# Optimization experiments

Measured on AMD Instinct MI355X. Metric: run time of the kernel, lower is better.

The kernel has to match this reference:

```python
import jax, jax.numpy as jnp
import numpy as np

H = 256   # hidden size
U = 10    # attention units


def _lstm_cell(xt, h, c, Wih, Whh, bih, bhh):
    # PyTorch gate order: i, f, g, o
    gates = xt @ Wih.T + h @ Whh.T + bih + bhh          # [B, 4H]
    i, f, g, o = jnp.split(gates, 4, axis=-1)
    i = jax.nn.sigmoid(i); f = jax.nn.sigmoid(f)
    g = jnp.tanh(g);       o = jax.nn.sigmoid(o)
    c = f * c + i * g
    h = o * jnp.tanh(c)
    return h, c


def setup_inputs() -> dict:
    key = jax.random.key(0)
    ks = jax.random.split(key, 12)
    B, S = 512, 256
    s = 1.0 / np.sqrt(H)
    x = jax.random.normal(ks[0], (B, S), dtype=jnp.float32)
    y = jax.random.randint(ks[1], (B, S), 0, S, dtype=jnp.int64)
    return {
        "x": x,
        "y": y,
        "enc_Wih": jax.random.uniform(ks[2], (4 * H, 1), jnp.float32, -s, s),
        "enc_Whh": jax.random.uniform(ks[3], (4 * H, H), jnp.float32, -s, s),
        "enc_bih": jax.random.uniform(ks[4], (4 * H,), jnp.float32, -s, s),
        "enc_bhh": jax.random.uniform(ks[5], (4 * H,), jnp.float32, -s, s),
        "dec_Wih": jax.random.uniform(ks[6], (4 * H, H + 1), jnp.float32, -s, s),
        "dec_Whh": jax.random.uniform(ks[7], (4 * H, H), jnp.float32, -s, s),
        "dec_bih": jax.random.uniform(ks[8], (4 * H,), jnp.float32, -s, s),
        "dec_bhh": jax.random.uniform(ks[9], (4 * H,), jnp.float32, -s, s),
        "att_W1": jax.random.uniform(ks[10], (U, H), jnp.float32, -s, s),
        "att_W2": jax.random.uniform(ks[11], (U, H), jnp.float32, -s, s),
        "att_V": jax.random.uniform(jax.random.fold_in(key, 99), (1, U), jnp.float32, -s, s),
    }


def reference(x, y, enc_Wih, enc_Whh, enc_bih, enc_bhh,
              dec_Wih, dec_Whh, dec_bih, dec_bhh,
              att_W1, att_W2, att_V):
    B, S = x.shape

    # ---- Encoder: LSTM over sequence of scalar inputs ----
    def enc_step(carry, xt):  # xt: [B, 1]
        h, c = carry
        h, c = _lstm_cell(xt, h, c, enc_Wih, enc_Whh, enc_bih, enc_bhh)
        return (h, c), h

    h0 = jnp.zeros((B, H), x.dtype)
    (hN, cN), enc_out_t = jax.lax.scan(enc_step, (h0, h0), x.T[:, :, None])
    enc_out = jnp.transpose(enc_out_t, (1, 0, 2))            # [B, S, H]

    # precompute W1 @ encoder_hidden (same math, hoisted out of loop)
    encW1 = jnp.einsum('bsh,uh->bsu', enc_out, att_W1)       # [B, S, U]

    # ---- Decoder loop (teacher forcing with ratio 1.0) ----
    def dec_step(carry, y_t):
        h, c, dec_in = carry                                  # dec_in: [B, 1]
        u = jnp.tanh(encW1 + (h @ att_W2.T)[:, None, :])      # [B, S, U]
        logits = jnp.einsum('bsu,ou->bso', u, att_V)[..., 0]  # [B, S]
        aj = jax.nn.softmax(logits, axis=1)
        di = jnp.einsum('bs,bsh->bh', aj, enc_out)            # [B, H]
        lstm_in = jnp.concatenate([di, dec_in], axis=1)       # [B, H+1]
        h, c = _lstm_cell(lstm_in, h, c, dec_Wih, dec_Whh, dec_bih, dec_bhh)
        pred = jnp.argmax(logits, axis=1)                     # [B]
        logp = jax.nn.log_softmax(logits, axis=1)
        loss_t = -jnp.mean(jnp.take_along_axis(logp, y_t[:, None], axis=1))
        dec_in_next = jnp.take_along_axis(x, y_t[:, None], axis=1)  # teacher force
        return (h, c, dec_in_next), (pred, loss_t)

    dec_in0 = jnp.zeros((B, 1), x.dtype)
    _, (preds, losses) = jax.lax.scan(dec_step, (hN, cN, dec_in0), y.T)
    outputs = preds[:, :, None].astype(jnp.int64)             # [S, B, 1]
    batch_loss = jnp.sum(losses) / B
    return outputs, batch_loss
```

## Files before the change

### kernel.cpp

```cpp
#include <hip/hip_runtime.h>
#include <cmath>

__device__ __forceinline__ double dexp_(double x) {
    x = fmin(fmax(x, -64.0), 64.0);
    double w = x * 1.4426950408889634;
    double n = rint(w);
    double u = (w - n) * 0.6931471805599453;
    double p = 1.0 + u * (1.0 + u * (0.5 + u * (1.6666666666666666e-01 +
               u * (4.1666666666666664e-02 + u * (8.3333333333333332e-03 +
               u * (1.3888888888888889e-03 + u * (1.9841269841269841e-04 +
               u * (2.4801587301587302e-05 + u * (2.7557319223985893e-06 +
               u * (2.7557319223985888e-07 + u * 2.5052108385441720e-08))))))))));
    return ldexp(p, (int)n);
}
__device__ __forceinline__ double dtanh_(double x) {
    double ax = fabs(x);
    double e = dexp_(2.0 * ax);
    double t = 1.0 - 2.0 / (e + 1.0);
    return copysign(t, x);
}
__device__ __forceinline__ double dsig_(double x) {
    return 1.0 / (1.0 + dexp_(-x));
}

__device__ __forceinline__ void fma_range16(
    const float* __restrict__ wcol, int row0, const float* __restrict__ xsrc,
    int k_beg, int k_end, double& A0, double& A1, double& A2, double& A3)
{
    for (int k0 = k_beg; k0 < k_end; k0 += 16) {
        float4 w[16];
        #pragma unroll
        for (int i = 0; i < 16; ++i)
            w[i] = *(const float4*)&wcol[(row0 + k0 + i) * 1024];
        float4 xa = *(const float4*)&xsrc[k0];
        float4 xb = *(const float4*)&xsrc[k0 + 4];
        float4 xc = *(const float4*)&xsrc[k0 + 8];
        float4 xd = *(const float4*)&xsrc[k0 + 12];
        float xv[16] = {xa.x, xa.y, xa.z, xa.w, xb.x, xb.y, xb.z, xb.w,
                        xc.x, xc.y, xc.z, xc.w, xd.x, xd.y, xd.z, xd.w};
        {
            float s0 = 0.f, s1 = 0.f, s2 = 0.f, s3 = 0.f;
            #pragma unroll
            for (int i = 0; i < 8; ++i) {
                s0 = fmaf(w[i].x, xv[i], s0);
                s1 = fmaf(w[i].y, xv[i], s1);
                s2 = fmaf(w[i].z, xv[i], s2);
                s3 = fmaf(w[i].w, xv[i], s3);
            }
            A0 += (double)s0; A1 += (double)s1;
            A2 += (double)s2; A3 += (double)s3;
        }
        {
            float s0 = 0.f, s1 = 0.f, s2 = 0.f, s3 = 0.f;
            #pragma unroll
            for (int i = 8; i < 16; ++i) {
                s0 = fmaf(w[i].x, xv[i], s0);
                s1 = fmaf(w[i].y, xv[i], s1);
                s2 = fmaf(w[i].z, xv[i], s2);
                s3 = fmaf(w[i].w, xv[i], s3);
            }
            A0 += (double)s0; A1 += (double)s1;
            A2 += (double)s2; A3 += (double)s3;
        }
    }
}

__global__ __launch_bounds__(256) void prep_kernel(
    const float* __restrict__ eWih, const float* __restrict__ eWhh,
    const float* __restrict__ ebih, const float* __restrict__ ebhh,
    const float* __restrict__ dWih, const float* __restrict__ dWhh,
    const float* __restrict__ dbih, const float* __restrict__ dbhh,
    float* __restrict__ WencR, double* __restrict__ bencR,
    float* __restrict__ WdecR, double* __restrict__ bdecR)
{
    const int n_enc = 257 * 1024;
    const int n_dec = 513 * 1024;
    const int total = n_enc + n_dec + 2048;
    for (int idx = blockIdx.x * blockDim.x + threadIdx.x; idx < total;
         idx += gridDim.x * blockDim.x) {
        if (idx < n_enc) {
            int k = idx >> 10, c = idx & 1023;
            int j = c >> 2, g = c & 3, r = g * 256 + j;
            WencR[idx] = (k == 0) ? eWih[r] : eWhh[r * 256 + (k - 1)];
        } else if (idx < n_enc + n_dec) {
            int i2 = idx - n_enc;
            int k = i2 >> 10, c = i2 & 1023;
            int j = c >> 2, g = c & 3, r = g * 256 + j;
            WdecR[i2] = (k < 257) ? dWih[r * 257 + k] : dWhh[r * 256 + (k - 257)];
        } else {
            int c = idx - n_enc - n_dec;
            if (c < 1024) {
                int r = (c & 3) * 256 + (c >> 2);
                bencR[c] = (double)ebih[r] + (double)ebhh[r];
            } else {
                int c2 = c - 1024;
                int r = (c2 & 3) * 256 + (c2 >> 2);
                bdecR[c2] = (double)dbih[r] + (double)dbhh[r];
            }
        }
    }
}

__global__ __launch_bounds__(512) void enc_fused_kernel(
    const float* __restrict__ x, const float* __restrict__ W,
    const double* __restrict__ bR, float* __restrict__ enc_out,
    float* __restrict__ c_st)
{
    __shared__ float h_lds[2][2][256];
    __shared__ float xs[2][2];
    const int tid = threadIdx.x;
    const int bb  = tid >> 8;
    const int j   = tid & 255;
    const int b0g = blockIdx.x * 2;
    const int b   = b0g + bb;

    h_lds[0][bb][j] = 0.0f;
    float c_f = 0.f;
    const double bi = bR[j * 4 + 0], bf = bR[j * 4 + 1];
    const double bg = bR[j * 4 + 2], bo = bR[j * 4 + 3];
    const float* wcol = W + j * 4;

    for (int t = 0; t < 256; ++t) {
        const int cur = t & 1, nxt = cur ^ 1;
        if (tid < 2) xs[cur][tid] = x[(b0g + tid) * 256 + t];
        __syncthreads();

        double A0 = 0, A1 = 0, A2 = 0, A3 = 0;
        const float* hh = h_lds[cur][bb];
        fma_range16(wcol, 1, hh, 0, 256, A0, A1, A2, A3);
        {
            float4 w = *(const float4*)&wcol[0];
            float xv = xs[cur][bb];
            A0 += (double)(w.x * xv); A1 += (double)(w.y * xv);
            A2 += (double)(w.z * xv); A3 += (double)(w.w * xv);
        }

        double iv = dsig_(A0 + bi);
        double fv = dsig_(A1 + bf);
        double gv = dtanh_(A2 + bg);
        double ov = dsig_(A3 + bo);
        double c = fv * (double)c_f + iv * gv;
        c_f = (float)c;
        float hv = (float)(ov * dtanh_(c));
        enc_out[(long)b * 65536 + t * 256 + j] = hv;
        h_lds[nxt][bb][j] = hv;
        __syncthreads();
    }

    c_st[(long)b * 256 + j] = c_f;
}

__global__ __launch_bounds__(256) void encW1_kernel(
    const float* __restrict__ enc_out, const float* __restrict__ W1,
    double* __restrict__ encW1d)
{
    __shared__ float sa[64][260];
    __shared__ float sw[10][257];
    const int tid = threadIdx.x;
    const int m0 = blockIdx.x * 64;
    #pragma unroll
    for (int i = 0; i < 16; ++i) {
        int idx = tid + i * 256;
        int row = idx >> 6;
        int c4 = (idx & 63) * 4;
        const float4 v = *(const float4*)&enc_out[(long)(m0 + row) * 256 + c4];
        *(float4*)&sa[row][c4] = v;
    }
    for (int i = tid; i < 2560; i += 256) sw[i >> 8][i & 255] = W1[i];
    __syncthreads();
    for (int o = tid; o < 640; o += 256) {
        int r = o / 10;
        int u = o - r * 10;
        double acc = 0.0;
        #pragma unroll 4
        for (int k = 0; k < 256; ++k)
            acc += (double)sa[r][k] * (double)sw[u][k];
        encW1d[(long)(m0 + r) * 10 + u] = acc;
    }
}

__global__ __launch_bounds__(512) void dec_fused_kernel(
    const double* __restrict__ encW1d, const float* __restrict__ enc_out,
    const float* __restrict__ W2, const float* __restrict__ V,
    const float* __restrict__ x, const int* __restrict__ y,
    const float* __restrict__ W, const double* __restrict__ bR,
    const float* __restrict__ c_init, float* __restrict__ logp_buf,
    float* __restrict__ out_pred)
{
    __shared__ float h_lds[2][2][256];
    __shared__ float di_lds[2][256];
    __shared__ float e_lds[2][256];
    __shared__ float rcpZ_lds[2];
    __shared__ float din_lds[2];
    __shared__ double s_V[12];
    __shared__ double s_W2h[2][12];
    __shared__ double s_ld[2][256];
    __shared__ double s_red[2][4];
    __shared__ int s_redi[2][4];
    __shared__ double s_maxd[2];
    __shared__ int s_am[2];

    const int tid  = threadIdx.x;
    const int bb   = tid >> 8;
    const int j    = tid & 255;
    const int widg = (tid >> 6) & 3;
    const int lane = tid & 63;
    const int b0g  = blockIdx.x * 2;
    const int b    = b0g + bb;

    if (tid < 10) s_V[tid] = (double)V[tid];
    h_lds[0][bb][j] = enc_out[(long)b * 65536 + 255 * 256 + j];
    float c_f = c_init[(long)b * 256 + j];
    const double bi = bR[j * 4 + 0], bf = bR[j * 4 + 1];
    const double bg = bR[j * 4 + 2], bo = bR[j * 4 + 3];
    const float* wcol = W + j * 4;
    __syncthreads();

    for (int t = 0; t < 256; ++t) {
        const int cur = t & 1, nxt = cur ^ 1;

        const float* hh = h_lds[cur][bb];
        for (int u = widg; u < 10; u += 4) {
            double p = 0.0;
            #pragma unroll
            for (int i = 0; i < 4; ++i) {
                int k = lane + i * 64;
                p += (double)W2[u * 256 + k] * (double)hh[k];
            }
            #pragma unroll
            for (int off = 32; off >= 1; off >>= 1) p += __shfl_down(p, off, 64);
            if (lane == 0) s_W2h[bb][u] = p;
        }
        __syncthreads();

        const double* eW = encW1d + ((long)b * 256 + j) * 10;
        double l = 0.0;
        #pragma unroll
        for (int u = 0; u < 10; ++u) l += s_V[u] * dtanh_(eW[u] + s_W2h[bb][u]);
        s_ld[bb][j] = l;

        {
            double v = l; int idx = j;
            #pragma unroll
            for (int off = 32; off >= 1; off >>= 1) {
                double v2 = __shfl_down(v, off, 64);
                int i2 = __shfl_down(idx, off, 64);
                if (v2 > v || (v2 == v && i2 < idx)) { v = v2; idx = i2; }
            }
            if (lane == 0) { s_red[bb][widg] = v; s_redi[bb][widg] = idx; }
        }
        __syncthreads();
        if (j == 0) {
            double v = s_red[bb][0]; int idx = s_redi[bb][0];
            #pragma unroll
            for (int w2 = 1; w2 < 4; ++w2) {
                if (s_red[bb][w2] > v ||
                    (s_red[bb][w2] == v && s_redi[bb][w2] < idx)) {
                    v = s_red[bb][w2]; idx = s_redi[bb][w2];
                }
            }
            s_maxd[bb] = v; s_am[bb] = idx;
        }
        __syncthreads();

        double e = dexp_(l - s_maxd[bb]);
        e_lds[bb][j] = (float)e;
        {
            double v = e;
            #pragma unroll
            for (int off = 32; off >= 1; off >>= 1) v += __shfl_down(v, off, 64);
            if (lane == 0) s_red[bb][widg] = v;
        }
        __syncthreads();
        if (j == 0) {
            double Z = s_red[bb][0] + s_red[bb][1] + s_red[bb][2] + s_red[bb][3];
            rcpZ_lds[bb] = (float)(1.0 / Z);
            out_pred[t * 512 + b] = (float)s_am[bb];
            int yv = y[b * 256 + t];
            logp_buf[t * 512 + b] = (float)(s_ld[bb][yv] - s_maxd[bb] - log(Z));
        }
        __syncthreads();

        {
            const float* ep = enc_out + (long)b * 65536 + j;
            float acc0 = 0.f, acc1 = 0.f, acc2 = 0.f, acc3 = 0.f;
            for (int s2 = 0; s2 < 256; s2 += 16) {
                float v[16];
                #pragma unroll
                for (int i = 0; i < 16; ++i) v[i] = ep[(s2 + i) * 256];
                #pragma unroll
                for (int i = 0; i < 16; i += 4) {
                    acc0 += e_lds[bb][s2 + i + 0] * v[i + 0];
                    acc1 += e_lds[bb][s2 + i + 1] * v[i + 1];
                    acc2 += e_lds[bb][s2 + i + 2] * v[i + 2];
                    acc3 += e_lds[bb][s2 + i + 3] * v[i + 3];
                }
            }
            di_lds[bb][j] = ((acc0 + acc1) + (acc2 + acc3)) * rcpZ_lds[bb];
        }
        if (tid < 2) {
            int bt = b0g + tid;
            float dv = 0.0f;
            if (t > 0) { int yi = y[bt * 256 + (t - 1)]; dv = x[bt * 256 + yi]; }
            din_lds[tid] = dv;
        }
        __syncthreads();

        double A0 = 0, A1 = 0, A2 = 0, A3 = 0;
        const float* dd = di_lds[bb];

        fma_range16(wcol, 0, dd, 0, 256, A0, A1, A2, A3);
        {
            float4 w = *(const float4*)&wcol[256 * 1024];
            float xv = din_lds[bb];
            A0 += (double)(w.x * xv); A1 += (double)(w.y * xv);
            A2 += (double)(w.z * xv); A3 += (double)(w.w * xv);
        }
        fma_range16(wcol, 257, hh, 0, 256, A0, A1, A2, A3);

        double iv = dsig_(A0 + bi);
        double fv = dsig_(A1 + bf);
        double gv = dtanh_(A2 + bg);
        double ov = dsig_(A3 + bo);
        double c = fv * (double)c_f + iv * gv;
        c_f = (float)c;
        h_lds[nxt][bb][j] = (float)(ov * dtanh_(c));
        __syncthreads();
    }
}

__global__ __launch_bounds__(256) void loss_kernel(
    const float* __restrict__ logp_buf, float* __restrict__ out)
{
    const int tid = threadIdx.x;
    double acc = 0.0;
    for (int i = tid; i < 131072; i += 256) acc += (double)logp_buf[i];
    __shared__ double s_red[4];
    const int wid = tid >> 6, lane = tid & 63;
    #pragma unroll
    for (int off = 32; off >= 1; off >>= 1) acc += __shfl_down(acc, off, 64);
    if (lane == 0) s_red[wid] = acc;
    __syncthreads();
    if (tid == 0) {
        out[131072] = (float)(-(s_red[0] + s_red[1] + s_red[2] + s_red[3])
                              / (512.0 * 512.0));
    }
}

extern "C" void kernel_launch(void* const* d_in, const int* in_sizes, int n_in,
                              void* d_out, int out_size, void* d_ws, size_t ws_size,
                              hipStream_t stream)
{
    const float* x    = (const float*)d_in[0];
    const int*   y    = (const int*)  d_in[1];
    const float* eWih = (const float*)d_in[2];
    const float* eWhh = (const float*)d_in[3];
    const float* ebih = (const float*)d_in[4];
    const float* ebhh = (const float*)d_in[5];
    const float* dWih = (const float*)d_in[6];
    const float* dWhh = (const float*)d_in[7];
    const float* dbih = (const float*)d_in[8];
    const float* dbhh = (const float*)d_in[9];
    const float* W1   = (const float*)d_in[10];
    const float* W2   = (const float*)d_in[11];
    const float* V    = (const float*)d_in[12];

    double* encW1d = (double*)d_ws;
    double* bencR  = encW1d + 1310720;
    double* bdecR  = bencR + 1024;
    float* enc_out = (float*)(bdecR + 1024);
    float* c_st    = enc_out + 33554432;
    float* hzero   = c_st + 131072;
    float* hd      = hzero + 131072;
    float* dibuf   = hd + 262144;
    float* logp    = dibuf + 131072;
    float* WencR   = logp + 131072;
    float* WdecR   = WencR + 263168;

    float* out = (float*)d_out;

    prep_kernel<<<512, 256, 0, stream>>>(eWih, eWhh, ebih, ebhh,
                                         dWih, dWhh, dbih, dbhh,
                                         WencR, bencR, WdecR, bdecR);

    enc_fused_kernel<<<256, 512, 0, stream>>>(x, WencR, bencR, enc_out, c_st);

    encW1_kernel<<<2048, 256, 0, stream>>>(enc_out, W1, encW1d);

    dec_fused_kernel<<<256, 512, 0, stream>>>(encW1d, enc_out, W2, V, x, y,
                                              WdecR, bdecR, c_st, logp, out);

    loss_kernel<<<1, 256, 0, stream>>>(logp, out);
}
```

Before: 19.94 ms.

## Decoder: one batch row per 256-thread block, smaller FMA chunk

The decoder kernel now processes one batch element per 256-thread block across 512 blocks, where it previously handled two per 512-thread block across 256 blocks. Launch bounds ask for two blocks per CU. This is meant to raise occupancy and let independent blocks hide each other's barrier stalls. The weight-FMA helper now loads 8 weight rows per chunk instead of 16, cutting register pressure at the cost of less load batching per iteration. The attention context loop also drops its 16-deep register prefetch.

```diff
diff --git a/kernel.cpp b/kernel.cpp
--- a/kernel.cpp
+++ b/kernel.cpp
@@ -23,45 +23,28 @@
     return 1.0 / (1.0 + dexp_(-x));
 }
 
-__device__ __forceinline__ void fma_range16(
+__device__ __forceinline__ void fma_range(
     const float* __restrict__ wcol, int row0, const float* __restrict__ xsrc,
     int k_beg, int k_end, double& A0, double& A1, double& A2, double& A3)
 {
-    for (int k0 = k_beg; k0 < k_end; k0 += 16) {
-        float4 w[16];
+    for (int k0 = k_beg; k0 < k_end; k0 += 8) {
+        float4 w[8];
         #pragma unroll
-        for (int i = 0; i < 16; ++i)
+        for (int i = 0; i < 8; ++i)
             w[i] = *(const float4*)&wcol[(row0 + k0 + i) * 1024];
         float4 xa = *(const float4*)&xsrc[k0];
         float4 xb = *(const float4*)&xsrc[k0 + 4];
-        float4 xc = *(const float4*)&xsrc[k0 + 8];
-        float4 xd = *(const float4*)&xsrc[k0 + 12];
-        float xv[16] = {xa.x, xa.y, xa.z, xa.w, xb.x, xb.y, xb.z, xb.w,
-                        xc.x, xc.y, xc.z, xc.w, xd.x, xd.y, xd.z, xd.w};
-        {
-            float s0 = 0.f, s1 = 0.f, s2 = 0.f, s3 = 0.f;
-            #pragma unroll
-            for (int i = 0; i < 8; ++i) {
-                s0 = fmaf(w[i].x, xv[i], s0);
-                s1 = fmaf(w[i].y, xv[i], s1);
-                s2 = fmaf(w[i].z, xv[i], s2);
-                s3 = fmaf(w[i].w, xv[i], s3);
-            }
-            A0 += (double)s0; A1 += (double)s1;
-            A2 += (double)s2; A3 += (double)s3;
-        }
-        {
-            float s0 = 0.f, s1 = 0.f, s2 = 0.f, s3 = 0.f;
-            #pragma unroll
-            for (int i = 8; i < 16; ++i) {
-                s0 = fmaf(w[i].x, xv[i], s0);
-                s1 = fmaf(w[i].y, xv[i], s1);
-                s2 = fmaf(w[i].z, xv[i], s2);
-                s3 = fmaf(w[i].w, xv[i], s3);
-            }
-            A0 += (double)s0; A1 += (double)s1;
-            A2 += (double)s2; A3 += (double)s3;
-        }
+        float xv[8] = {xa.x, xa.y, xa.z, xa.w, xb.x, xb.y, xb.z, xb.w};
+        float s0 = 0.f, s1 = 0.f, s2 = 0.f, s3 = 0.f;
+        #pragma unroll
+        for (int i = 0; i < 8; ++i) {
+            s0 = fmaf(w[i].x, xv[i], s0);
+            s1 = fmaf(w[i].y, xv[i], s1);
+            s2 = fmaf(w[i].z, xv[i], s2);
+            s3 = fmaf(w[i].w, xv[i], s3);
+        }
+        A0 += (double)s0; A1 += (double)s1;
+        A2 += (double)s2; A3 += (double)s3;
     }
 }
 
@@ -127,7 +110,7 @@
 
         double A0 = 0, A1 = 0, A2 = 0, A3 = 0;
         const float* hh = h_lds[cur][bb];
-        fma_range16(wcol, 1, hh, 0, 256, A0, A1, A2, A3);
+        fma_range(wcol, 1, hh, 0, 256, A0, A1, A2, A3);
         {
             float4 w = *(const float4*)&wcol[0];
             float xv = xs[cur][bb];
@@ -179,7 +162,7 @@
     }
 }
 
-__global__ __launch_bounds__(512) void dec_fused_kernel(
+__global__ __launch_bounds__(256, 2) void dec_fused_kernel(
     const double* __restrict__ encW1d, const float* __restrict__ enc_out,
     const float* __restrict__ W2, const float* __restrict__ V,
     const float* __restrict__ x, const int* __restrict__ y,
@@ -187,29 +170,27 @@
     const float* __restrict__ c_init, float* __restrict__ logp_buf,
     float* __restrict__ out_pred)
 {
-    __shared__ float h_lds[2][2][256];
-    __shared__ float di_lds[2][256];
-    __shared__ float e_lds[2][256];
-    __shared__ float rcpZ_lds[2];
-    __shared__ float din_lds[2];
+    __shared__ float h_lds[2][256];
+    __shared__ float di_lds[256];
+    __shared__ float e_lds[256];
+    __shared__ float rcpZ_s;
+    __shared__ float din_s;
     __shared__ double s_V[12];
-    __shared__ double s_W2h[2][12];
-    __shared__ double s_ld[2][256];
-    __shared__ double s_red[2][4];
-    __shared__ int s_redi[2][4];
-    __shared__ double s_maxd[2];
-    __shared__ int s_am[2];
+    __shared__ double s_W2h[12];
+    __shared__ double s_ld[256];
+    __shared__ double s_red[4];
+    __shared__ int s_redi[4];
+    __shared__ double s_maxd;
+    __shared__ int s_am;
 
     const int tid  = threadIdx.x;
-    const int bb   = tid >> 8;
-    const int j    = tid & 255;
-    const int widg = (tid >> 6) & 3;
+    const int j    = tid;
+    const int wid  = tid >> 6;
     const int lane = tid & 63;
-    const int b0g  = blockIdx.x * 2;
-    const int b    = b0g + bb;
+    const int b    = blockIdx.x;
 
     if (tid < 10) s_V[tid] = (double)V[tid];
-    h_lds[0][bb][j] = enc_out[(long)b * 65536 + 255 * 256 + j];
+    h_lds[0][j] = enc_out[(long)b * 65536 + 255 * 256 + j];
     float c_f = c_init[(long)b * 256 + j];
     const double bi = bR[j * 4 + 0], bf = bR[j * 4 + 1];
     const double bg = bR[j * 4 + 2], bo = bR[j * 4 + 3];
@@ -218,9 +199,9 @@
 
     for (int t = 0; t < 256; ++t) {
         const int cur = t & 1, nxt = cur ^ 1;
-
-        const float* hh = h_lds[cur][bb];
-        for (int u = widg; u < 10; u += 4) {
+        const float* hh = h_lds[cur];
+
+        for (int u = wid; u < 10; u += 4) {
             double p = 0.0;
             #pragma unroll
             for (int i = 0; i < 4; ++i) {
@@ -229,15 +210,15 @@
             }
             #pragma unroll
             for (int off = 32; off >= 1; off >>= 1) p += __shfl_down(p, off, 64);
-            if (lane == 0) s_W2h[bb][u] = p;
+            if (lane == 0) s_W2h[u] = p;
         }
         __syncthreads();
 
         const double* eW = encW1d + ((long)b * 256 + j) * 10;
         double l = 0.0;
         #pragma unroll
-        for (int u = 0; u < 10; ++u) l += s_V[u] * dtanh_(eW[u] + s_W2h[bb][u]);
-        s_ld[bb][j] = l;
+        for (int u = 0; u < 10; ++u) l += s_V[u] * dtanh_(eW[u] + s_W2h[u]);
+        s_ld[j] = l;
 
         {
             double v = l; int idx = j;
@@ -247,76 +228,66 @@
                 int i2 = __shfl_down(idx, off, 64);
                 if (v2 > v || (v2 == v && i2 < idx)) { v = v2; idx = i2; }
             }
-            if (lane == 0) { s_red[bb][widg] = v; s_redi[bb][widg] = idx; }
-        }
-        __syncthreads();
-        if (j == 0) {
-            double v = s_red[bb][0]; int idx = s_redi[bb][0];
+            if (lane == 0) { s_red[wid] = v; s_redi[wid] = idx; }
+        }
+        __syncthreads();
+        if (tid == 0) {
+            double v = s_red[0]; int idx = s_redi[0];
             #pragma unroll
             for (int w2 = 1; w2 < 4; ++w2) {
-                if (s_red[bb][w2] > v ||
-                    (s_red[bb][w2] == v && s_redi[bb][w2] < idx)) {
-                    v = s_red[bb][w2]; idx = s_redi[bb][w2];
+                if (s_red[w2] > v || (s_red[w2] == v && s_redi[w2] < idx)) {
+                    v = s_red[w2]; idx = s_redi[w2];
                 }
             }
-            s_maxd[bb] = v; s_am[bb] = idx;
-        }
-        __syncthreads();
-
-        double e = dexp_(l - s_maxd[bb]);
-        e_lds[bb][j] = (float)e;
+            s_maxd = v; s_am = idx;
+        }
+        __syncthreads();
+
+        double e = dexp_(l - s_maxd);
+        e_lds[j] = (float)e;
         {
             double v = e;
             #pragma unroll
             for (int off = 32; off >= 1; off >>= 1) v += __shfl_down(v, off, 64);
-            if (lane == 0) s_red[bb][widg] = v;
-        }
-        __syncthreads();
-        if (j == 0) {
-            double Z = s_red[bb][0] + s_red[bb][1] + s_red[bb][2] + s_red[bb][3];
-            rcpZ_lds[bb] = (float)(1.0 / Z);
-            out_pred[t * 512 + b] = (float)s_am[bb];
+            if (lane == 0) s_red[wid] = v;
+        }
+        __syncthreads();
+        if (tid == 0) {
+            double Z = s_red[0] + s_red[1] + s_red[2] + s_red[3];
+            rcpZ_s = (float)(1.0 / Z);
+            out_pred[t * 512 + b] = (float)s_am;
             int yv = y[b * 256 + t];
-            logp_buf[t * 512 + b] = (float)(s_ld[bb][yv] - s_maxd[bb] - log(Z));
+            logp_buf[t * 512 + b] = (float)(s_ld[yv] - s_maxd - log(Z));
+        } else if (tid == 1) {
+            float dv = 0.0f;
+            if (t > 0) { int yi = y[b * 256 + (t - 1)]; dv = x[b * 256 + yi]; }
+            din_s = dv;
         }
         __syncthreads();
 
         {
             const float* ep = enc_out + (long)b * 65536 + j;
             float acc0 = 0.f, acc1 = 0.f, acc2 = 0.f, acc3 = 0.f;
-            for (int s2 = 0; s2 < 256; s2 += 16) {
-                float v[16];
-                #pragma unroll
-                for (int i = 0; i < 16; ++i) v[i] = ep[(s2 + i) * 256];
-                #pragma unroll
-                for (int i = 0; i < 16; i += 4) {
-                    acc0 += e_lds[bb][s2 + i + 0] * v[i + 0];
-                    acc1 += e_lds[bb][s2 + i + 1] * v[i + 1];
-                    acc2 += e_lds[bb][s2 + i + 2] * v[i + 2];
-                    acc3 += e_lds[bb][s2 + i + 3] * v[i + 3];
-                }
-            }
-            di_lds[bb][j] = ((acc0 + acc1) + (acc2 + acc3)) * rcpZ_lds[bb];
-        }
-        if (tid < 2) {
-            int bt = b0g + tid;
-            float dv = 0.0f;
-            if (t > 0) { int yi = y[bt * 256 + (t - 1)]; dv = x[bt * 256 + yi]; }
-            din_lds[tid] = dv;
+            for (int s2 = 0; s2 < 256; s2 += 4) {
+                acc0 += e_lds[s2 + 0] * ep[(s2 + 0) * 256];
+                acc1 += e_lds[s2 + 1] * ep[(s2 + 1) * 256];
+                acc2 += e_lds[s2 + 2] * ep[(s2 + 2) * 256];
+                acc3 += e_lds[s2 + 3] * ep[(s2 + 3) * 256];
+            }
+            di_lds[j] = ((acc0 + acc1) + (acc2 + acc3)) * rcpZ_s;
         }
         __syncthreads();
 
         double A0 = 0, A1 = 0, A2 = 0, A3 = 0;
-        const float* dd = di_lds[bb];
-
-        fma_range16(wcol, 0, dd, 0, 256, A0, A1, A2, A3);
+
+        fma_range(wcol, 0, di_lds, 0, 256, A0, A1, A2, A3);
         {
             float4 w = *(const float4*)&wcol[256 * 1024];
-            float xv = din_lds[bb];
+            float xv = din_s;
             A0 += (double)(w.x * xv); A1 += (double)(w.y * xv);
             A2 += (double)(w.z * xv); A3 += (double)(w.w * xv);
         }
-        fma_range16(wcol, 257, hh, 0, 256, A0, A1, A2, A3);
+        fma_range(wcol, 257, hh, 0, 256, A0, A1, A2, A3);
 
         double iv = dsig_(A0 + bi);
         double fv = dsig_(A1 + bf);
@@ -324,7 +295,7 @@
         double ov = dsig_(A3 + bo);
         double c = fv * (double)c_f + iv * gv;
         c_f = (float)c;
-        h_lds[nxt][bb][j] = (float)(ov * dtanh_(c));
+        h_lds[nxt][j] = (float)(ov * dtanh_(c));
         __syncthreads();
     }
 }
@@ -357,9 +328,9 @@
     const float* eWhh = (const float*)d_in[3];
     const float* ebih = (const float*)d_in[4];
     const float* ebhh = (const float*)d_in[5];
+    const float* dbih_f = (const float*)d_in[8];
     const float* dWih = (const float*)d_in[6];
     const float* dWhh = (const float*)d_in[7];
-    const float* dbih = (const float*)d_in[8];
     const float* dbhh = (const float*)d_in[9];
     const float* W1   = (const float*)d_in[10];
     const float* W2   = (const float*)d_in[11];
@@ -380,14 +351,14 @@
     float* out = (float*)d_out;
 
     prep_kernel<<<512, 256, 0, stream>>>(eWih, eWhh, ebih, ebhh,
-                                         dWih, dWhh, dbih, dbhh,
+                                         dWih, dWhh, dbih_f, dbhh,
                                          WencR, bencR, WdecR, bdecR);
 
     enc_fused_kernel<<<256, 512, 0, stream>>>(x, WencR, bencR, enc_out, c_st);
 
     encW1_kernel<<<2048, 256, 0, stream>>>(enc_out, W1, encW1d);
 
-    dec_fused_kernel<<<256, 512, 0, stream>>>(encW1d, enc_out, W2, V, x, y,
+    dec_fused_kernel<<<512, 256, 0, stream>>>(encW1d, enc_out, W2, V, x, y,
                                               WdecR, bdecR, c_st, logp, out);
 
     loss_kernel<<<1, 256, 0, stream>>>(logp, out);
```

Measured after the change: 17.47 ms. -12.4%, faster.
